# Kernel optimization log

Hardware: AMD Instinct MI355X
Metric: run time of the kernel (lower is better)

The kernel has to match this reference:

```python
import jax, jax.numpy as jnp
import numpy as np

ATOMS_PER_RES = 24  # hard-coded in .view(B, N_l, -1, 24)
NEG_SLOPE = 0.01    # nn.LeakyReLU default


def setup_inputs() -> dict:
    key = jax.random.key(0)
    ks = jax.random.split(key, 10)
    B, N_l, N_p, H, G = 16, 64, 512, 128, 10
    pos_l = jax.random.normal(ks[0], (B, N_l, 3), jnp.float32) * 5.0
    pos_p = jax.random.normal(ks[1], (B, N_p, ATOMS_PER_RES, 3), jnp.float32) * 5.0
    Interact = jax.random.normal(ks[2], (B, N_l, N_p, H), jnp.float32)
    Interact_mask = jax.random.randint(ks[3], (B, N_l, N_p), 0, 2) > 0
    W_pi = jax.random.normal(ks[4], (H, G), jnp.float32) * 0.05
    b_pi = jnp.zeros((G,), jnp.float32)
    W_sigma = jax.random.normal(ks[5], (H, G), jnp.float32) * 0.05
    b_sigma = jnp.zeros((G,), jnp.float32)
    W_mu = jax.random.normal(ks[6], (H, G), jnp.float32) * 0.05
    b_mu = jnp.zeros((G,), jnp.float32)
    return {
        "pos_l": pos_l, "pos_p": pos_p, "Interact": Interact,
        "Interact_mask": Interact_mask,
        "W_pi": W_pi, "b_pi": b_pi,
        "W_sigma": W_sigma, "b_sigma": b_sigma,
        "W_mu": W_mu, "b_mu": b_mu,
    }


def _min_dist(pos_l, pos_p):
    # pos_l: [B, N_l, 3]; pos_p: [B, N_p, 24, 3]
    B, N_l, _ = pos_l.shape
    Y = pos_p.reshape(B, -1, 3)  # [B, N_p*24, 3]
    d2 = (jnp.sum(pos_l * pos_l, axis=-1)[..., None]
          + jnp.sum(Y * Y, axis=-1)[:, None, :]
          - 2.0 * jnp.einsum('bic,bjc->bij', pos_l, Y))  # [B, N_l, N_p*24]
    dist = jnp.nan_to_num(jnp.sqrt(d2), nan=10000.0)
    # min over the 24 atoms of each residue -> [B, N_l, N_p]
    return dist.reshape(B, N_l, -1, ATOMS_PER_RES).min(axis=-1)


def reference(pos_l, pos_p, Interact, Interact_mask,
              W_pi, b_pi, W_sigma, b_sigma, W_mu, b_mu):
    leaky = lambda x: jax.nn.leaky_relu(x, NEG_SLOPE)
    dist = _min_dist(pos_l, pos_p)                       # [B, N_l, N_p]
    # original gathers dist[Interact_mask]; keep static shape, zero-fill masked-out
    dist_masked = jnp.where(Interact_mask, dist, 0.0)
    pi = jax.nn.softmax(Interact @ W_pi + b_pi, axis=-1)          # [B,N_l,N_p,G]
    sigma = jnp.clip(leaky(Interact @ W_sigma + b_sigma) + 1.1, 1e-6, None)
    mu = leaky(Interact @ W_mu + b_mu) + 1.0
    return pi, sigma, mu, dist_masked, Interact_mask
```

## Files before the change

### kernel.cpp

```cpp
#include <hip/hip_runtime.h>
#include <cmath>

#define NB 16
#define NL 64
#define NP 512
#define NH 128
#define NG 10
#define ROWS (NB * NL * NP)

#define OFF_PI    ((size_t)0)
#define OFF_SIGMA ((size_t)5242880)
#define OFF_MU    ((size_t)10485760)
#define OFF_DIST  ((size_t)15728640)
#define OFF_MASK  ((size_t)16252928)

typedef __attribute__((ext_vector_type(8))) short short8;
typedef __attribute__((ext_vector_type(4))) float f32x4;

__device__ __forceinline__ unsigned pk2(float a, float b) {
    unsigned ua = __float_as_uint(a);
    unsigned ub = __float_as_uint(b);
    ua = (ua + 0x7fffu + ((ua >> 16) & 1u)) >> 16;
    ub = (ub + 0x7fffu + ((ub >> 16) & 1u)) & 0xffff0000u;
    return ua | ub;
}

__global__ __launch_bounds__(256, 3) void k_fused(
    const float* __restrict__ pos_l,
    const float* __restrict__ pos_p,
    const int*   __restrict__ mask,
    const float* __restrict__ X,
    const float* __restrict__ Wpi, const float* __restrict__ bpi,
    const float* __restrict__ Wsg, const float* __restrict__ bsg,
    const float* __restrict__ Wmu, const float* __restrict__ bmu,
    float* __restrict__ out_pi,
    float* __restrict__ out_sg,
    float* __restrict__ out_mu,
    float* __restrict__ dist_out,
    float* __restrict__ mask_out)
{
    __shared__ __align__(16) float cs[4 * 64 * 36];

    const int tid  = threadIdx.x;
    const int wv   = tid >> 6;
    const int lane = tid & 63;
    const int lrow = lane & 15;
    const int lkg  = lane >> 4;
    const int idx  = blockIdx.x * 256 + tid;
    const size_t row0 = (size_t)blockIdx.x * 256;

    {
        int p  = idx & (NP - 1);
        int bl = idx >> 9;
        int b  = bl >> 6;

        const float* xl = pos_l + bl * 3;
        float x0 = xl[0], x1 = xl[1], x2 = xl[2];
        float qs = x0 * x0 + x1 * x1 + x2 * x2;

        const float4* yp = (const float4*)(pos_p + ((size_t)(b * NP + p)) * 72);

        float m2 = 1e30f;
        #pragma unroll
        for (int q = 0; q < 6; ++q) {
            float4 v0 = yp[q * 3 + 0];
            float4 v1 = yp[q * 3 + 1];
            float4 v2 = yp[q * 3 + 2];
            float c[12] = {v0.x, v0.y, v0.z, v0.w,
                           v1.x, v1.y, v1.z, v1.w,
                           v2.x, v2.y, v2.z, v2.w};
            #pragma unroll
            for (int a = 0; a < 4; ++a) {
                float yx = c[a * 3 + 0], yy = c[a * 3 + 1], yz = c[a * 3 + 2];
                float d2 = qs + (yx * yx + yy * yy + yz * yz)
                              - 2.0f * (x0 * yx + x1 * yy + x2 * yz);
                d2 = (d2 >= 0.0f) ? d2 : 1e8f;
                m2 = fminf(m2, d2);
            }
        }
        float m = sqrtf(m2);
        int mk = mask[idx];
        dist_out[idx] = mk ? m : 0.0f;
        mask_out[idx] = mk ? 1.0f : 0.0f;
    }

    const int c0 = lrow;
    const int c1 = lrow + 16;
    const float* wb0; float bv0;
    if (c0 < 10) { wb0 = Wpi + c0;      bv0 = bpi[c0]; }
    else         { wb0 = Wsg + c0 - 10; bv0 = bsg[c0 - 10]; }
    const float* wb1; float bv1; bool pad1;
    if (c1 < 20)      { wb1 = Wsg + c1 - 10; bv1 = bsg[c1 - 10]; pad1 = false; }
    else if (c1 < 30) { wb1 = Wmu + c1 - 20; bv1 = bmu[c1 - 20]; pad1 = false; }
    else              { wb1 = Wpi;           bv1 = 0.0f;         pad1 = true; }

    f32x4 acc[4][2];
    #pragma unroll
    for (int m = 0; m < 4; ++m) {
        acc[m][0] = (f32x4){bv0, bv0, bv0, bv0};
        acc[m][1] = (f32x4){bv1, bv1, bv1, bv1};
    }

    const float* xbase = X + (row0 + wv * 64 + lrow) * NH + lkg * 8;

    #pragma unroll 1
    for (int ks = 0; ks < 4; ++ks) {
        const int kb = ks * 32 + lkg * 8;
        float w0[8], w1[8];
        #pragma unroll
        for (int j = 0; j < 8; ++j) {
            w0[j] = wb0[(kb + j) * NG];
            float t = wb1[(kb + j) * NG];
            w1[j] = pad1 ? 0.0f : t;
        }
        uint4 u0 = {pk2(w0[0], w0[1]), pk2(w0[2], w0[3]),
                    pk2(w0[4], w0[5]), pk2(w0[6], w0[7])};
        uint4 u1 = {pk2(w1[0], w1[1]), pk2(w1[2], w1[3]),
                    pk2(w1[4], w1[5]), pk2(w1[6], w1[7])};
        short8 bf0 = __builtin_bit_cast(short8, u0);
        short8 bf1 = __builtin_bit_cast(short8, u1);

        #pragma unroll
        for (int m = 0; m < 4; ++m) {
            const float* ap = xbase + (size_t)m * 16 * NH + ks * 32;
            float4 lo = *(const float4*)ap;
            float4 hi = *(const float4*)(ap + 4);
            uint4 ua = {pk2(lo.x, lo.y), pk2(lo.z, lo.w),
                        pk2(hi.x, hi.y), pk2(hi.z, hi.w)};
            short8 af = __builtin_bit_cast(short8, ua);
            acc[m][0] = __builtin_amdgcn_mfma_f32_16x16x32_bf16(af, bf0, acc[m][0], 0, 0, 0);
            acc[m][1] = __builtin_amdgcn_mfma_f32_16x16x32_bf16(af, bf1, acc[m][1], 0, 0, 0);
        }
    }

    float* cw = cs + wv * (64 * 36);
    #pragma unroll
    for (int m = 0; m < 4; ++m)
        #pragma unroll
        for (int n = 0; n < 2; ++n)
            #pragma unroll
            for (int r = 0; r < 4; ++r)
                cw[(m * 16 + lkg * 4 + r) * 36 + n * 16 + lrow] = acc[m][n][r];

    const float* myrow = cs + wv * (64 * 36) + lane * 36;
    float a[32];
    #pragma unroll
    for (int j = 0; j < 8; ++j)
        *(float4*)&a[4 * j] = *(const float4*)&myrow[4 * j];

    const size_t ro = (size_t)idx * NG;

    float mx = a[0];
    #pragma unroll
    for (int g = 1; g < NG; ++g) mx = fmaxf(mx, a[g]);
    float e[NG], ssum = 0.0f;
    #pragma unroll
    for (int g = 0; g < NG; ++g) { e[g] = __expf(a[g] - mx); ssum += e[g]; }
    float inv = 1.0f / ssum;
    #pragma unroll
    for (int g = 0; g < 5; ++g)
        *(float2*)&out_pi[ro + 2 * g] = make_float2(e[2 * g] * inv,
                                                    e[2 * g + 1] * inv);

    #pragma unroll
    for (int g = 0; g < 5; ++g) {
        float xa = a[10 + 2 * g], xb = a[10 + 2 * g + 1];
        float va = fmaxf((xa >= 0.0f ? xa : 0.01f * xa) + 1.1f, 1e-6f);
        float vb = fmaxf((xb >= 0.0f ? xb : 0.01f * xb) + 1.1f, 1e-6f);
        *(float2*)&out_sg[ro + 2 * g] = make_float2(va, vb);
    }

    #pragma unroll
    for (int g = 0; g < 5; ++g) {
        float xa = a[20 + 2 * g], xb = a[20 + 2 * g + 1];
        float va = (xa >= 0.0f ? xa : 0.01f * xa) + 1.0f;
        float vb = (xb >= 0.0f ? xb : 0.01f * xb) + 1.0f;
        *(float2*)&out_mu[ro + 2 * g] = make_float2(va, vb);
    }
}

extern "C" void kernel_launch(void* const* d_in, const int* in_sizes, int n_in,
                              void* d_out, int out_size, void* d_ws, size_t ws_size,
                              hipStream_t stream) {
    const float* pos_l    = (const float*)d_in[0];
    const float* pos_p    = (const float*)d_in[1];
    const float* Interact = (const float*)d_in[2];
    const int*   mask     = (const int*)  d_in[3];
    const float* Wpi      = (const float*)d_in[4];
    const float* bpi      = (const float*)d_in[5];
    const float* Wsg      = (const float*)d_in[6];
    const float* bsg      = (const float*)d_in[7];
    const float* Wmu      = (const float*)d_in[8];
    const float* bmu      = (const float*)d_in[9];

    float* out      = (float*)d_out;
    float* out_pi   = out + OFF_PI;
    float* out_sg   = out + OFF_SIGMA;
    float* out_mu   = out + OFF_MU;
    float* out_dist = out + OFF_DIST;
    float* out_mask = out + OFF_MASK;

    hipLaunchKernelGGL(k_fused, dim3(ROWS / 256), dim3(256), 0, stream,
                       pos_l, pos_p, mask, Interact,
                       Wpi, bpi, Wsg, bsg, Wmu, bmu,
                       out_pi, out_sg, out_mu, out_dist, out_mask);
}
```

Measured before the change: 402.3 us.

## Prefetch Interact tiles and weights before distance compute, double-buffer K loop

Weight loads and the first K-slice of the Interact tile are issued before the min-distance computation, so their latency overlaps the distance work. The MFMA K loop is fully unrolled with register double-buffering that prefetches the next slice, and all weights are converted to bf16 once up front. The hand-written bf16 packing is replaced with the library __float2bfloat16 conversion. This raises register pressure under the 3-blocks-per-SM launch bound, which could force spills or lower occupancy.

```diff
diff --git a/kernel.cpp b/kernel.cpp
--- a/kernel.cpp
+++ b/kernel.cpp
@@ -1,4 +1,5 @@
 #include <hip/hip_runtime.h>
+#include <hip/hip_bf16.h>
 #include <cmath>
 
 #define NB 16
@@ -17,12 +18,8 @@
 typedef __attribute__((ext_vector_type(8))) short short8;
 typedef __attribute__((ext_vector_type(4))) float f32x4;
 
-__device__ __forceinline__ unsigned pk2(float a, float b) {
-    unsigned ua = __float_as_uint(a);
-    unsigned ub = __float_as_uint(b);
-    ua = (ua + 0x7fffu + ((ua >> 16) & 1u)) >> 16;
-    ub = (ub + 0x7fffu + ((ub >> 16) & 1u)) & 0xffff0000u;
-    return ua | ub;
+__device__ __forceinline__ short bfc(float x) {
+    return (short)__builtin_bit_cast(unsigned short, __float2bfloat16(x));
 }
 
 __global__ __launch_bounds__(256, 3) void k_fused(
@@ -49,41 +46,6 @@
     const int idx  = blockIdx.x * 256 + tid;
     const size_t row0 = (size_t)blockIdx.x * 256;
 
-    {
-        int p  = idx & (NP - 1);
-        int bl = idx >> 9;
-        int b  = bl >> 6;
-
-        const float* xl = pos_l + bl * 3;
-        float x0 = xl[0], x1 = xl[1], x2 = xl[2];
-        float qs = x0 * x0 + x1 * x1 + x2 * x2;
-
-        const float4* yp = (const float4*)(pos_p + ((size_t)(b * NP + p)) * 72);
-
-        float m2 = 1e30f;
-        #pragma unroll
-        for (int q = 0; q < 6; ++q) {
-            float4 v0 = yp[q * 3 + 0];
-            float4 v1 = yp[q * 3 + 1];
-            float4 v2 = yp[q * 3 + 2];
-            float c[12] = {v0.x, v0.y, v0.z, v0.w,
-                           v1.x, v1.y, v1.z, v1.w,
-                           v2.x, v2.y, v2.z, v2.w};
-            #pragma unroll
-            for (int a = 0; a < 4; ++a) {
-                float yx = c[a * 3 + 0], yy = c[a * 3 + 1], yz = c[a * 3 + 2];
-                float d2 = qs + (yx * yx + yy * yy + yz * yz)
-                              - 2.0f * (x0 * yx + x1 * yy + x2 * yz);
-                d2 = (d2 >= 0.0f) ? d2 : 1e8f;
-                m2 = fminf(m2, d2);
-            }
-        }
-        float m = sqrtf(m2);
-        int mk = mask[idx];
-        dist_out[idx] = mk ? m : 0.0f;
-        mask_out[idx] = mk ? 1.0f : 0.0f;
-    }
-
     const int c0 = lrow;
     const int c1 = lrow + 16;
     const float* wb0; float bv0;
@@ -94,6 +56,73 @@
     else if (c1 < 30) { wb1 = Wmu + c1 - 20; bv1 = bmu[c1 - 20]; pad1 = false; }
     else              { wb1 = Wpi;           bv1 = 0.0f;         pad1 = true; }
 
+    float w0v[32], w1v[32];
+    #pragma unroll
+    for (int ks = 0; ks < 4; ++ks)
+        #pragma unroll
+        for (int j = 0; j < 8; ++j) {
+            int k = ks * 32 + lkg * 8 + j;
+            w0v[ks * 8 + j] = wb0[k * NG];
+            w1v[ks * 8 + j] = wb1[k * NG];
+        }
+
+    const float* xbase = X + (row0 + wv * 64 + lrow) * NH + lkg * 8;
+    float4 xc0[4], xc1[4];
+    #pragma unroll
+    for (int m = 0; m < 4; ++m) {
+        const float* ap = xbase + (size_t)m * 16 * NH;
+        xc0[m] = *(const float4*)ap;
+        xc1[m] = *(const float4*)(ap + 4);
+    }
+
+    {
+        int p  = idx & (NP - 1);
+        int bl = idx >> 9;
+        int b  = bl >> 6;
+
+        const float* xl = pos_l + bl * 3;
+        float x0 = xl[0], x1 = xl[1], x2 = xl[2];
+        float qs = x0 * x0 + x1 * x1 + x2 * x2;
+
+        const float4* yp = (const float4*)(pos_p + ((size_t)(b * NP + p)) * 72);
+
+        float m2 = 1e30f;
+        #pragma unroll
+        for (int q = 0; q < 6; ++q) {
+            float4 v0 = yp[q * 3 + 0];
+            float4 v1 = yp[q * 3 + 1];
+            float4 v2 = yp[q * 3 + 2];
+            float c[12] = {v0.x, v0.y, v0.z, v0.w,
+                           v1.x, v1.y, v1.z, v1.w,
+                           v2.x, v2.y, v2.z, v2.w};
+            #pragma unroll
+            for (int a = 0; a < 4; ++a) {
+                float yx = c[a * 3 + 0], yy = c[a * 3 + 1], yz = c[a * 3 + 2];
+                float d2 = qs + (yx * yx + yy * yy + yz * yz)
+                              - 2.0f * (x0 * yx + x1 * yy + x2 * yz);
+                d2 = (d2 >= 0.0f) ? d2 : 1e8f;
+                m2 = fminf(m2, d2);
+            }
+        }
+        float m = sqrtf(m2);
+        int mk = mask[idx];
+        dist_out[idx] = mk ? m : 0.0f;
+        mask_out[idx] = mk ? 1.0f : 0.0f;
+    }
+
+    short8 bf0[4], bf1[4];
+    #pragma unroll
+    for (int ks = 0; ks < 4; ++ks) {
+        short8 t0, t1;
+        #pragma unroll
+        for (int j = 0; j < 8; ++j) {
+            t0[j] = bfc(w0v[ks * 8 + j]);
+            t1[j] = pad1 ? (short)0 : bfc(w1v[ks * 8 + j]);
+        }
+        bf0[ks] = t0;
+        bf1[ks] = t1;
+    }
+
     f32x4 acc[4][2];
     #pragma unroll
     for (int m = 0; m < 4; ++m) {
@@ -101,35 +130,31 @@
         acc[m][1] = (f32x4){bv1, bv1, bv1, bv1};
     }
 
-    const float* xbase = X + (row0 + wv * 64 + lrow) * NH + lkg * 8;
-
-    #pragma unroll 1
+    float4 xn0[4], xn1[4];
+    #pragma unroll
     for (int ks = 0; ks < 4; ++ks) {
-        const int kb = ks * 32 + lkg * 8;
-        float w0[8], w1[8];
-        #pragma unroll
-        for (int j = 0; j < 8; ++j) {
-            w0[j] = wb0[(kb + j) * NG];
-            float t = wb1[(kb + j) * NG];
-            w1[j] = pad1 ? 0.0f : t;
-        }
-        uint4 u0 = {pk2(w0[0], w0[1]), pk2(w0[2], w0[3]),
-                    pk2(w0[4], w0[5]), pk2(w0[6], w0[7])};
-        uint4 u1 = {pk2(w1[0], w1[1]), pk2(w1[2], w1[3]),
-                    pk2(w1[4], w1[5]), pk2(w1[6], w1[7])};
-        short8 bf0 = __builtin_bit_cast(short8, u0);
-        short8 bf1 = __builtin_bit_cast(short8, u1);
-
+        if (ks < 3) {
+            #pragma unroll
+            for (int m = 0; m < 4; ++m) {
+                const float* ap = xbase + (size_t)m * 16 * NH + (ks + 1) * 32;
+                xn0[m] = *(const float4*)ap;
+                xn1[m] = *(const float4*)(ap + 4);
+            }
+        }
         #pragma unroll
         for (int m = 0; m < 4; ++m) {
-            const float* ap = xbase + (size_t)m * 16 * NH + ks * 32;
-            float4 lo = *(const float4*)ap;
-            float4 hi = *(const float4*)(ap + 4);
-            uint4 ua = {pk2(lo.x, lo.y), pk2(lo.z, lo.w),
-                        pk2(hi.x, hi.y), pk2(hi.z, hi.w)};
-            short8 af = __builtin_bit_cast(short8, ua);
-            acc[m][0] = __builtin_amdgcn_mfma_f32_16x16x32_bf16(af, bf0, acc[m][0], 0, 0, 0);
-            acc[m][1] = __builtin_amdgcn_mfma_f32_16x16x32_bf16(af, bf1, acc[m][1], 0, 0, 0);
+            float c[8] = {xc0[m].x, xc0[m].y, xc0[m].z, xc0[m].w,
+                          xc1[m].x, xc1[m].y, xc1[m].z, xc1[m].w};
+            short8 af;
+            #pragma unroll
+            for (int j = 0; j < 8; ++j) af[j] = bfc(c[j]);
+            acc[m][0] = __builtin_amdgcn_mfma_f32_16x16x32_bf16(af, bf0[ks], acc[m][0], 0, 0, 0);
+            acc[m][1] = __builtin_amdgcn_mfma_f32_16x16x32_bf16(af, bf1[ks], acc[m][1], 0, 0, 0);
+        }
+        #pragma unroll
+        for (int m = 0; m < 4; ++m) {
+            xc0[m] = xn0[m];
+            xc1[m] = xn1[m];
         }
     }
 
```

Result: slower. 421.4 us (+4.8%).

## Prepack bf16 weight fragments and software-pipeline activation loads ahead of MFMA

Applied to the files above, without the earlier changes.

Adds a small pre-kernel that packs the three weight matrices into a bf16 MFMA fragment table in workspace, so the main kernel loads ready-made B fragments instead of doing strided scalar weight loads and bf16 conversion per block. The main kernel now issues its first activation tile loads before the distance computation and double-buffers the next 16-row tile while running MFMAs on the current one. The goal is to hide global load latency on this memory-bound kernel. In exchange it uses more registers per thread under the 3-block occupancy bound, and adds one extra tiny kernel launch.

```diff
diff --git a/kernel.cpp b/kernel.cpp
--- a/kernel.cpp
+++ b/kernel.cpp
@@ -25,14 +25,40 @@
     return ua | ub;
 }
 
+__global__ __launch_bounds__(512) void k_pack(
+    const float* __restrict__ Wpi, const float* __restrict__ Wsg,
+    const float* __restrict__ Wmu, uint4* __restrict__ tbl)
+{
+    int e    = threadIdx.x;
+    int lane = e & 63;
+    int n    = (e >> 6) & 1;
+    int ks   = e >> 7;
+    int lrow = lane & 15, lkg = lane >> 4;
+    int col  = n * 16 + lrow;
+    float w[8];
+    #pragma unroll
+    for (int j = 0; j < 8; ++j) {
+        int k = ks * 32 + lkg * 8 + j;
+        float v = 0.0f;
+        if      (col < 10) v = Wpi[k * NG + col];
+        else if (col < 20) v = Wsg[k * NG + col - 10];
+        else if (col < 30) v = Wmu[k * NG + col - 20];
+        w[j] = v;
+    }
+    uint4 u = {pk2(w[0], w[1]), pk2(w[2], w[3]),
+               pk2(w[4], w[5]), pk2(w[6], w[7])};
+    tbl[e] = u;
+}
+
 __global__ __launch_bounds__(256, 3) void k_fused(
     const float* __restrict__ pos_l,
     const float* __restrict__ pos_p,
     const int*   __restrict__ mask,
     const float* __restrict__ X,
-    const float* __restrict__ Wpi, const float* __restrict__ bpi,
-    const float* __restrict__ Wsg, const float* __restrict__ bsg,
-    const float* __restrict__ Wmu, const float* __restrict__ bmu,
+    const uint4* __restrict__ wtbl,
+    const float* __restrict__ bpi,
+    const float* __restrict__ bsg,
+    const float* __restrict__ bmu,
     float* __restrict__ out_pi,
     float* __restrict__ out_sg,
     float* __restrict__ out_mu,
@@ -48,6 +74,23 @@
     const int lkg  = lane >> 4;
     const int idx  = blockIdx.x * 256 + tid;
     const size_t row0 = (size_t)blockIdx.x * 256;
+
+    uint4 bu0[4], bu1[4];
+    #pragma unroll
+    for (int ks = 0; ks < 4; ++ks) {
+        bu0[ks] = wtbl[(ks * 2 + 0) * 64 + lane];
+        bu1[ks] = wtbl[(ks * 2 + 1) * 64 + lane];
+    }
+
+    const int c0 = lrow, c1 = lrow + 16;
+    const float bv0 = (c0 < 10) ? bpi[c0] : bsg[c0 - 10];
+    const float bv1 = (c1 < 20) ? bsg[c1 - 10] : (c1 < 30 ? bmu[c1 - 20] : 0.0f);
+
+    const float* xbase = X + (row0 + wv * 64 + lrow) * NH + lkg * 8;
+    float4 xc[8], xn[8];
+    #pragma unroll
+    for (int q = 0; q < 8; ++q)
+        xc[q] = *(const float4*)(xbase + (q >> 1) * 32 + (q & 1) * 4);
 
     {
         int p  = idx & (NP - 1);
@@ -84,16 +127,6 @@
         mask_out[idx] = mk ? 1.0f : 0.0f;
     }
 
-    const int c0 = lrow;
-    const int c1 = lrow + 16;
-    const float* wb0; float bv0;
-    if (c0 < 10) { wb0 = Wpi + c0;      bv0 = bpi[c0]; }
-    else         { wb0 = Wsg + c0 - 10; bv0 = bsg[c0 - 10]; }
-    const float* wb1; float bv1; bool pad1;
-    if (c1 < 20)      { wb1 = Wsg + c1 - 10; bv1 = bsg[c1 - 10]; pad1 = false; }
-    else if (c1 < 30) { wb1 = Wmu + c1 - 20; bv1 = bmu[c1 - 20]; pad1 = false; }
-    else              { wb1 = Wpi;           bv1 = 0.0f;         pad1 = true; }
-
     f32x4 acc[4][2];
     #pragma unroll
     for (int m = 0; m < 4; ++m) {
@@ -101,36 +134,27 @@
         acc[m][1] = (f32x4){bv1, bv1, bv1, bv1};
     }
 
-    const float* xbase = X + (row0 + wv * 64 + lrow) * NH + lkg * 8;
-
-    #pragma unroll 1
-    for (int ks = 0; ks < 4; ++ks) {
-        const int kb = ks * 32 + lkg * 8;
-        float w0[8], w1[8];
-        #pragma unroll
-        for (int j = 0; j < 8; ++j) {
-            w0[j] = wb0[(kb + j) * NG];
-            float t = wb1[(kb + j) * NG];
-            w1[j] = pad1 ? 0.0f : t;
+    #pragma unroll
+    for (int m = 0; m < 4; ++m) {
+        if (m < 3) {
+            const float* ap = xbase + (size_t)(m + 1) * 16 * NH;
+            #pragma unroll
+            for (int q = 0; q < 8; ++q)
+                xn[q] = *(const float4*)(ap + (q >> 1) * 32 + (q & 1) * 4);
         }
-        uint4 u0 = {pk2(w0[0], w0[1]), pk2(w0[2], w0[3]),
-                    pk2(w0[4], w0[5]), pk2(w0[6], w0[7])};
-        uint4 u1 = {pk2(w1[0], w1[1]), pk2(w1[2], w1[3]),
-                    pk2(w1[4], w1[5]), pk2(w1[6], w1[7])};
-        short8 bf0 = __builtin_bit_cast(short8, u0);
-        short8 bf1 = __builtin_bit_cast(short8, u1);
-
-        #pragma unroll
-        for (int m = 0; m < 4; ++m) {
-            const float* ap = xbase + (size_t)m * 16 * NH + ks * 32;
-            float4 lo = *(const float4*)ap;
-            float4 hi = *(const float4*)(ap + 4);
+        #pragma unroll
+        for (int ks = 0; ks < 4; ++ks) {
+            float4 lo = xc[ks * 2], hi = xc[ks * 2 + 1];
             uint4 ua = {pk2(lo.x, lo.y), pk2(lo.z, lo.w),
                         pk2(hi.x, hi.y), pk2(hi.z, hi.w)};
             short8 af = __builtin_bit_cast(short8, ua);
-            acc[m][0] = __builtin_amdgcn_mfma_f32_16x16x32_bf16(af, bf0, acc[m][0], 0, 0, 0);
-            acc[m][1] = __builtin_amdgcn_mfma_f32_16x16x32_bf16(af, bf1, acc[m][1], 0, 0, 0);
+            acc[m][0] = __builtin_amdgcn_mfma_f32_16x16x32_bf16(
+                af, __builtin_bit_cast(short8, bu0[ks]), acc[m][0], 0, 0, 0);
+            acc[m][1] = __builtin_amdgcn_mfma_f32_16x16x32_bf16(
+                af, __builtin_bit_cast(short8, bu1[ks]), acc[m][1], 0, 0, 0);
         }
+        #pragma unroll
+        for (int q = 0; q < 8; ++q) xc[q] = xn[q];
     }
 
     float* cw = cs + wv * (64 * 36);
@@ -200,8 +224,12 @@
     float* out_dist = out + OFF_DIST;
     float* out_mask = out + OFF_MASK;
 
+    uint4* wtbl = (uint4*)d_ws;
+
+    hipLaunchKernelGGL(k_pack, dim3(1), dim3(512), 0, stream,
+                       Wpi, Wsg, Wmu, wtbl);
     hipLaunchKernelGGL(k_fused, dim3(ROWS / 256), dim3(256), 0, stream,
-                       pos_l, pos_p, mask, Interact,
-                       Wpi, bpi, Wsg, bsg, Wmu, bmu,
+                       pos_l, pos_p, mask, Interact, wtbl,
+                       bpi, bsg, bmu,
                        out_pi, out_sg, out_mu, out_dist, out_mask);
 }
```

Result: slower. 410.9 us (+2.1%).
